# Performance work log

Measured on AMD Instinct MI355X. Metric: run time of the kernel, lower is better.

The kernel has to match this reference:

```python
import jax, jax.numpy as jnp
import numpy as np

N_MENTIONS = 4096
N_PAIRS = 32768
N_SEGMENTS = 1024  # number of spans (ragged softmax groups)
G_DIM = 3 * 768    # span representation dim (3*embed_dim)
D_IN = 3 * G_DIM + 20
HIDDEN = 150


def setup_inputs() -> dict:
    key = jax.random.key(0)
    ks = jax.random.split(key, 11)
    inp = {
        "g_i": jax.random.normal(ks[0], (N_MENTIONS, G_DIM), jnp.float32),
        "mention_scores": jax.random.normal(ks[1], (N_MENTIONS, 1), jnp.float32),
        "speaker_embed": jax.random.normal(ks[2], (3, 20), jnp.float32) * 0.02,
        "W1": jax.random.normal(ks[3], (D_IN, HIDDEN), jnp.float32) * (1.0 / np.sqrt(D_IN)),
        "b1": jnp.zeros((HIDDEN,), jnp.float32),
        "W2": jax.random.normal(ks[4], (HIDDEN, 1), jnp.float32) * (1.0 / np.sqrt(HIDDEN)),
        "b2": jnp.zeros((1,), jnp.float32),
        "mention_ids": jax.random.randint(ks[5], (N_PAIRS,), 0, N_MENTIONS),
        "antecedent_ids": jax.random.randint(ks[6], (N_PAIRS,), 0, N_MENTIONS),
        "speaker_labels": jax.random.randint(ks[7], (N_PAIRS,), 0, 3),
        "segment_ids": jnp.sort(jax.random.randint(ks[8], (N_PAIRS,), 0, N_SEGMENTS)),
    }
    return inp


def reference(g_i, mention_scores, speaker_embed, W1, b1, W2, b2,
              mention_ids, antecedent_ids, speaker_labels, segment_ids):
    # Gather mention / antecedent span representations. [P, G]
    i_g = g_i[mention_ids]
    j_g = g_i[antecedent_ids]
    phi = speaker_embed[speaker_labels]  # [P, speaker_dim]

    # Pair features: cat(i_g, j_g, i_g*j_g, phi). [P, D_IN]
    pairs = jnp.concatenate([i_g, j_g, i_g * j_g, phi], axis=1)

    # Score MLP: Linear -> ReLU -> Linear(->1). (dropout off in eval)
    h = jax.nn.relu(pairs @ W1 + b1)          # [P, HIDDEN]
    s_ij = (h @ W2 + b2)[:, 0]                # [P]

    # coref score = s_i + s_j + s_ij
    s_i = mention_scores[mention_ids, 0]
    s_j = mention_scores[antecedent_ids, 0]
    scores = s_i + s_j + s_ij                 # [P]

    # Ragged per-span softmax with an appended epsilon logit of 0.0.
    seg_max = jax.ops.segment_max(scores, segment_ids, num_segments=N_SEGMENTS)
    m = jnp.maximum(seg_max, 0.0)             # include epsilon=0 in the max
    e = jnp.exp(scores - m[segment_ids])      # [P]
    eps_e = jnp.exp(-m)                       # [S] exp(0 - m)
    denom = jax.ops.segment_sum(e, segment_ids, num_segments=N_SEGMENTS) + eps_e
    pair_probs = e / denom[segment_ids]       # [P]
    eps_probs = eps_e / denom                 # [S]

    # Flattened: all pair probs followed by the per-span epsilon probs.
    return jnp.concatenate([pair_probs, eps_probs])
```

## Files before the change

kernel.cpp:

```cpp
#include <hip/hip_runtime.h>
#include <cstdint>

#define NM   4096
#define NP   32768
#define NSEG 1024
#define GD   2304
#define HID  150
#define NPAD 160
#define KG32 72
#define SEG_ELEMS (KG32 * 10 * 512)

typedef unsigned short u16;
typedef short s16x8 __attribute__((ext_vector_type(8)));
typedef float f32x4 __attribute__((ext_vector_type(4)));
typedef uint32_t u32x4 __attribute__((ext_vector_type(4)));

union Frag {
    uint32_t u[4];
    s16x8    v;
};

__device__ inline uint32_t cvtpk(float lo, float hi) {
    uint32_t r;
    asm("v_cvt_pk_bf16_f32 %0, %1, %2" : "=v"(r) : "v"(lo), "v"(hi));
    return r;
}

__device__ inline f32x4 mfma16(s16x8 a, s16x8 b, f32x4 c) {
    return __builtin_amdgcn_mfma_f32_16x16x32_bf16(a, b, c, 0, 0, 0);
}

__device__ inline s16x8 prodpack(u32x4 iu, u32x4 ju) {
    Frag f;
#pragma unroll
    for (int m = 0; m < 4; ++m) {
        uint32_t x = iu[m], y = ju[m];
        float lo = __builtin_bit_cast(float, x << 16) *
                   __builtin_bit_cast(float, y << 16);
        float hi = __builtin_bit_cast(float, x & 0xffff0000u) *
                   __builtin_bit_cast(float, y & 0xffff0000u);
        f.u[m] = cvtpk(lo, hi);
    }
    return f.v;
}

__global__ void prep_pack_kernel(const float* __restrict__ W1,
                                 u16* __restrict__ wpack) {
    int idx = blockIdx.x * 256 + threadIdx.x;
    if (idx >= 3 * KG32 * 10 * 64) return;
    int lane = idx & 63;
    int t    = idx >> 6;
    int nf   = t % 10;
    int sk   = t / 10;
    int seg  = sk / KG32, kg = sk % KG32;
    int kbase = (seg == 0) ? 2 * GD : ((seg == 1) ? 0 : GD);
    int n    = nf * 16 + (lane & 15);
    int krow = kbase + kg * 32 + ((lane >> 4) << 3);
    u32x4 d = (u32x4){0u, 0u, 0u, 0u};
    if (n < HID) {
#pragma unroll
        for (int jj = 0; jj < 4; ++jj) {
            float v0 = W1[(size_t)(krow + 2 * jj) * HID + n];
            float v1 = W1[(size_t)(krow + 2 * jj + 1) * HID + n];
            d[jj] = cvtpk(v0, v1);
        }
    }
    *(u32x4*)(wpack + (size_t)idx * 8) = d;
}

__global__ void prep_tables_kernel(const float* __restrict__ spk,
                                   const float* __restrict__ W1,
                                   const float* __restrict__ b1,
                                   const float* __restrict__ W2,
                                   float* __restrict__ phib,
                                   float* __restrict__ w2pad) {
    int t = threadIdx.x;
    if (t < 3 * NPAD) {
        int s = t / NPAD, n = t - s * NPAD;
        float a = 0.f;
        if (n < HID) {
            for (int d = 0; d < 20; ++d)
                a = fmaf(spk[s * 20 + d], W1[(size_t)(3 * GD + d) * HID + n], a);
            a += b1[n];
        }
        phib[t] = a;
    } else if (t < 4 * NPAD) {
        int n = t - 3 * NPAD;
        w2pad[n] = (n < HID) ? W2[n] : 0.f;
    }
}

struct A2 { f32x4 x0, x1; };

__launch_bounds__(256)
__global__ void gemm_pre_kernel(const float* __restrict__ gi,
                                const u16* __restrict__ wpackIJ,
                                u16* __restrict__ gbf,
                                float* __restrict__ APre) {
    const int tid = threadIdx.x;
    const int kh = tid >> 6, lane = tid & 63;
    const int quad = lane >> 4, l15 = lane & 15;
    const int mt = blockIdx.x, ng = blockIdx.y;
    const u16* wp = wpackIJ + (size_t)ng * SEG_ELEMS + lane * 8;
    const int row = mt * 16 + l15;

    __shared__ float xch[3][64][44];

    f32x4 acc[10];
#pragma unroll
    for (int b = 0; b < 10; ++b) acc[b] = (f32x4){0.f, 0.f, 0.f, 0.f};

    const float* ap = gi + (size_t)row * GD + quad * 8;
    u16* gb = gbf + (size_t)row * GD + quad * 8;
    const bool emit = (ng == 0);
    const int u0 = kh * 18;

    A2 a0, a1, a2;
    Frag b0[10], b1[10];

#define LDA(ax, k) { ax.x0 = *(const f32x4*)(ap + (u0 + (k)) * 32); \
                     ax.x1 = *(const f32x4*)(ap + (u0 + (k)) * 32 + 4); }
#define LDBP(bb, k) { const u16* wn = wp + (size_t)(u0 + (k)) * 5120; \
        _Pragma("unroll") for (int nf = 0; nf < 10; ++nf) \
            bb[nf].v = *(const s16x8*)(const void*)(wn + nf * 512); }
#define PHP(k, ax, bb) { \
        Frag a; \
        a.u[0] = cvtpk(ax.x0[0], ax.x0[1]); a.u[1] = cvtpk(ax.x0[2], ax.x0[3]); \
        a.u[2] = cvtpk(ax.x1[0], ax.x1[1]); a.u[3] = cvtpk(ax.x1[2], ax.x1[3]); \
        if (emit) *(u32x4*)(gb + (u0 + (k)) * 32) = *(const u32x4*)a.u; \
        __builtin_amdgcn_s_setprio(1); \
        _Pragma("unroll") for (int nf = 0; nf < 10; ++nf) \
            acc[nf] = mfma16(a.v, bb[nf].v, acc[nf]); \
        __builtin_amdgcn_s_setprio(0); }

    LDBP(b0, 0); LDBP(b1, 1);
    LDA(a0, 0); LDA(a1, 1); LDA(a2, 2);

#pragma unroll 1
    for (int t = 0; t < 2; ++t) {
        const int kb = t * 6;
        PHP(kb + 0, a0, b0); LDBP(b0, kb + 2); LDA(a0, kb + 3);
        PHP(kb + 1, a1, b1); LDBP(b1, kb + 3); LDA(a1, kb + 4);
        PHP(kb + 2, a2, b0); LDBP(b0, kb + 4); LDA(a2, kb + 5);
        PHP(kb + 3, a0, b1); LDBP(b1, kb + 5); LDA(a0, kb + 6);
        PHP(kb + 4, a1, b0); LDBP(b0, kb + 6); LDA(a1, kb + 7);
        PHP(kb + 5, a2, b1); LDBP(b1, kb + 7); LDA(a2, kb + 8);
    }
    PHP(12, a0, b0); LDBP(b0, 14); LDA(a0, 15);
    PHP(13, a1, b1); LDBP(b1, 15); LDA(a1, 16);
    PHP(14, a2, b0); LDBP(b0, 16); LDA(a2, 17);
    PHP(15, a0, b1); LDBP(b1, 17);
    PHP(16, a1, b0);
    PHP(17, a2, b1);

#undef LDA
#undef LDBP
#undef PHP

    if (kh != 0) {
        float* dst = &xch[kh - 1][lane][0];
#pragma unroll
        for (int nf = 0; nf < 10; ++nf)
            *(f32x4*)(dst + nf * 4) = acc[nf];
    }
    __syncthreads();
    if (kh == 0) {
#pragma unroll
        for (int k = 0; k < 3; ++k) {
            const float* src = &xch[k][lane][0];
#pragma unroll
            for (int nf = 0; nf < 10; ++nf)
                acc[nf] += *(const f32x4*)(src + nf * 4);
        }
        const int colbase = ng * NPAD + l15;
        float* Ap = APre + (size_t)(mt * 16 + quad * 4) * 320 + colbase;
#pragma unroll
        for (int nf = 0; nf < 10; ++nf)
#pragma unroll
            for (int r = 0; r < 4; ++r)
                Ap[(size_t)r * 320 + nf * 16] = acc[nf][r];
    }
}

struct G4 { u32x4 i0, j0, i1, j1; };

__launch_bounds__(128)
__global__ void gemm_pairs_kernel(const u16* __restrict__ gbf,
                                  const u16* __restrict__ wpackP,
                                  const float* __restrict__ APre,
                                  const float* __restrict__ phib,
                                  const float* __restrict__ w2pad,
                                  const float* __restrict__ mscore,
                                  const float* __restrict__ b2,
                                  const int* __restrict__ mids,
                                  const int* __restrict__ aids,
                                  const int* __restrict__ slab,
                                  float* __restrict__ scores) {
    const int tid = threadIdx.x;
    const int wave = tid >> 6, lane = tid & 63;
    const int quad = lane >> 4, l15 = lane & 15;
    const int base = blockIdx.x * 64 + wave * 32;

    f32x4 acc[2][10];
#pragma unroll
    for (int a = 0; a < 2; ++a)
#pragma unroll
        for (int b = 0; b < 10; ++b) acc[a][b] = (f32x4){0.f, 0.f, 0.f, 0.f};

    const int p0 = base + l15, p1 = base + 16 + l15;
    const u16* ip0 = gbf + (size_t)mids[p0] * GD + quad * 8;
    const u16* jp0 = gbf + (size_t)aids[p0] * GD + quad * 8;
    const u16* ip1 = gbf + (size_t)mids[p1] * GD + quad * 8;
    const u16* jp1 = gbf + (size_t)aids[p1] * GD + quad * 8;
    const u16* wl = wpackP + lane * 8;

    G4 g0, g1, g2, g3;
    Frag b0[10], b1[10];

#define LDG(g, k) { const int off = (k) * 32; \
        g.i0 = *(const u32x4*)(ip0 + off); g.j0 = *(const u32x4*)(jp0 + off); \
        g.i1 = *(const u32x4*)(ip1 + off); g.j1 = *(const u32x4*)(jp1 + off); }
#define LDB(bb, k) { const u16* wn = wl + (size_t)(k) * 5120; \
        _Pragma("unroll") for (int nf = 0; nf < 10; ++nf) \
            bb[nf].v = *(const s16x8*)(const void*)(wn + nf * 512); }
#define PH(g, bb) { \
        s16x8 a0 = prodpack(g.i0, g.j0); \
        s16x8 a1 = prodpack(g.i1, g.j1); \
        __builtin_amdgcn_s_setprio(1); \
        _Pragma("unroll") for (int nf = 0; nf < 10; ++nf) { \
            acc[0][nf] = mfma16(a0, bb[nf].v, acc[0][nf]); \
            acc[1][nf] = mfma16(a1, bb[nf].v, acc[1][nf]); } \
        __builtin_amdgcn_s_setprio(0); }

    LDB(b0, 0); LDB(b1, 1);
    LDG(g0, 0); LDG(g1, 1); LDG(g2, 2); LDG(g3, 3);

#pragma unroll 1
    for (int t = 0; t < 17; ++t) {
        const int kb = t * 4;
        PH(g0, b0); LDB(b0, kb + 2); LDG(g0, kb + 4);
        PH(g1, b1); LDB(b1, kb + 3); LDG(g1, kb + 5);
        PH(g2, b0); LDB(b0, kb + 4); LDG(g2, kb + 6);
        PH(g3, b1); LDB(b1, kb + 5); LDG(g3, kb + 7);
    }
    PH(g0, b0); LDB(b0, 70);
    PH(g1, b1); LDB(b1, 71);
    PH(g2, b0);
    PH(g3, b1);

#undef LDG
#undef LDB
#undef PH

    float w2v[10];
#pragma unroll
    for (int nf = 0; nf < 10; ++nf) w2v[nf] = w2pad[nf * 16 + l15];
    const float b2v = b2[0];

#pragma unroll
    for (int mf = 0; mf < 2; ++mf)
#pragma unroll
        for (int r = 0; r < 4; ++r) {
            const int p  = base + mf * 16 + quad * 4 + r;
            const int mi = mids[p], ai = aids[p], sp = slab[p];
            const float* Ai = APre + (size_t)mi * 320;
            const float* Bj = APre + (size_t)ai * 320 + NPAD;
            const float* Ph = phib + sp * NPAD;
            float partial = 0.f;
#pragma unroll
            for (int nf = 0; nf < 10; ++nf) {
                const int c = nf * 16 + l15;
                float h = acc[mf][nf][r] + Ai[c] + Bj[c] + Ph[c];
                h = fmaxf(h, 0.f);
                partial = fmaf(h, w2v[nf], partial);
            }
            partial += __shfl_xor(partial, 1);
            partial += __shfl_xor(partial, 2);
            partial += __shfl_xor(partial, 4);
            partial += __shfl_xor(partial, 8);
            if (l15 == 0)
                scores[p] = partial + b2v + mscore[mi] + mscore[ai];
        }
}

__global__ void seg_softmax_kernel(const float* __restrict__ scores,
                                   const int* __restrict__ seg,
                                   float* __restrict__ out) {
    const int s = blockIdx.x;
    const int lane = threadIdx.x;
    int lo = 0, hi = NP;
    while (lo < hi) { int mid = (lo + hi) >> 1; if (seg[mid] < s) lo = mid + 1; else hi = mid; }
    const int start = lo;
    int lo2 = start, hi2 = NP;
    while (lo2 < hi2) { int mid = (lo2 + hi2) >> 1; if (seg[mid] <= s) lo2 = mid + 1; else hi2 = mid; }
    const int end = lo2;

    float m = 0.f;
    for (int i = start + lane; i < end; i += 64) m = fmaxf(m, scores[i]);
#pragma unroll
    for (int msk = 1; msk < 64; msk <<= 1) m = fmaxf(m, __shfl_xor(m, msk));

    float sum = 0.f;
    for (int i = start + lane; i < end; i += 64) sum += __expf(scores[i] - m);
#pragma unroll
    for (int msk = 1; msk < 64; msk <<= 1) sum += __shfl_xor(sum, msk);

    const float epse = __expf(-m);
    const float inv  = 1.f / (sum + epse);
    for (int i = start + lane; i < end; i += 64) out[i] = __expf(scores[i] - m) * inv;
    if (lane == 0) out[NP + s] = epse * inv;
}

extern "C" void kernel_launch(void* const* d_in, const int* in_sizes, int n_in,
                              void* d_out, int out_size, void* d_ws, size_t ws_size,
                              hipStream_t stream) {
    const float* gi     = (const float*)d_in[0];
    const float* mscore = (const float*)d_in[1];
    const float* spk    = (const float*)d_in[2];
    const float* W1     = (const float*)d_in[3];
    const float* b1     = (const float*)d_in[4];
    const float* W2     = (const float*)d_in[5];
    const float* b2     = (const float*)d_in[6];
    const int*   mids   = (const int*)d_in[7];
    const int*   aids   = (const int*)d_in[8];
    const int*   slab   = (const int*)d_in[9];
    const int*   segs   = (const int*)d_in[10];
    float* out = (float*)d_out;

    char* w = (char*)d_ws;
    u16*   gbf    = (u16*)w;
    u16*   wpack  = (u16*)(w + 18874368);
    float* APre   = (float*)(w + 21086208);
    float* scores = (float*)(w + 26329088);
    float* phib   = (float*)(w + 26460160);
    float* w2pad  = (float*)(w + 26462080);

    prep_pack_kernel<<<dim3((3 * KG32 * 10 * 64 + 255) / 256), dim3(256), 0, stream>>>(W1, wpack);
    prep_tables_kernel<<<dim3(1), dim3(640), 0, stream>>>(spk, W1, b1, W2, phib, w2pad);
    gemm_pre_kernel<<<dim3(256, 2), dim3(256), 0, stream>>>(gi, wpack + SEG_ELEMS, gbf, APre);
    gemm_pairs_kernel<<<dim3(512), dim3(128), 0, stream>>>(gbf, wpack, APre, phib, w2pad,
                                                           mscore, b2, mids, aids, slab, scores);
    seg_softmax_kernel<<<dim3(NSEG), dim3(64), 0, stream>>>(scores, segs, out);
}
```

Measured before the change: 193.1 us.

## Bucket pairs by mention id, merge pre-GEMM halves, retune pair pipeline

Adds histogram, scan and scatter kernels that sort pair indices into 8 buckets by mention id. Each pair-GEMM block works within one bucket so gathered mention rows share L2 locality. The pre-GEMM now computes both the i and j projections in one block, reading g_i once instead of twice. It also drops the s_setprio hints and changes the pair kernel's prefetch depth from 4 to 3 stages with 6-step unrolling. Costs are three extra launches, atomics, higher register pressure in the fused pre-GEMM (launch bounds now 256,1), and some idle blocks because of the per-bucket padding.

```diff
diff --git a/kernel.cpp b/kernel.cpp
--- a/kernel.cpp
+++ b/kernel.cpp
@@ -9,6 +9,8 @@
 #define NPAD 160
 #define KG32 72
 #define SEG_ELEMS (KG32 * 10 * 512)
+#define NBUCK 8
+#define BUCK_SHIFT 9
 
 typedef unsigned short u16;
 typedef short s16x8 __attribute__((ext_vector_type(8)));
@@ -73,8 +75,10 @@
                                    const float* __restrict__ b1,
                                    const float* __restrict__ W2,
                                    float* __restrict__ phib,
-                                   float* __restrict__ w2pad) {
+                                   float* __restrict__ w2pad,
+                                   int* __restrict__ cnts) {
     int t = threadIdx.x;
+    if (t < 16) cnts[t] = 0;
     if (t < 3 * NPAD) {
         int s = t / NPAD, n = t - s * NPAD;
         float a = 0.f;
@@ -90,78 +94,115 @@
     }
 }
 
+__global__ void bucket_hist_kernel(const int* __restrict__ mids,
+                                   int* __restrict__ cnts) {
+    int p = blockIdx.x * 256 + threadIdx.x;
+    if (p < NP) atomicAdd(&cnts[mids[p] >> BUCK_SHIFT], 1);
+}
+
+__global__ void bucket_scan_kernel(int* __restrict__ cnts) {
+    if (threadIdx.x == 0) {
+        int base = 0;
+        for (int b = 0; b < NBUCK; ++b) {
+            int c = cnts[b];
+            cnts[8 + b] = base;
+            base += c;
+            cnts[b] = 0;
+        }
+    }
+}
+
+__global__ void bucket_scatter_kernel(const int* __restrict__ mids,
+                                      int* __restrict__ cnts,
+                                      int* __restrict__ perm) {
+    int p = blockIdx.x * 256 + threadIdx.x;
+    if (p < NP) {
+        int b = mids[p] >> BUCK_SHIFT;
+        int pos = cnts[8 + b] + atomicAdd(&cnts[b], 1);
+        perm[pos] = p;
+    }
+}
+
 struct A2 { f32x4 x0, x1; };
 
-__launch_bounds__(256)
+__launch_bounds__(256, 1)
 __global__ void gemm_pre_kernel(const float* __restrict__ gi,
-                                const u16* __restrict__ wpackIJ,
+                                const u16* __restrict__ wpack,
                                 u16* __restrict__ gbf,
                                 float* __restrict__ APre) {
     const int tid = threadIdx.x;
     const int kh = tid >> 6, lane = tid & 63;
     const int quad = lane >> 4, l15 = lane & 15;
-    const int mt = blockIdx.x, ng = blockIdx.y;
-    const u16* wp = wpackIJ + (size_t)ng * SEG_ELEMS + lane * 8;
+    const int mt = blockIdx.x;
+    const u16* wpi = wpack + (size_t)1 * SEG_ELEMS + lane * 8;
+    const u16* wpj = wpack + (size_t)2 * SEG_ELEMS + lane * 8;
     const int row = mt * 16 + l15;
 
-    __shared__ float xch[3][64][44];
-
-    f32x4 acc[10];
-#pragma unroll
-    for (int b = 0; b < 10; ++b) acc[b] = (f32x4){0.f, 0.f, 0.f, 0.f};
+    __shared__ float xch[3][64][88];
+
+    f32x4 acci[10], accj[10];
+#pragma unroll
+    for (int b = 0; b < 10; ++b) {
+        acci[b] = (f32x4){0.f, 0.f, 0.f, 0.f};
+        accj[b] = (f32x4){0.f, 0.f, 0.f, 0.f};
+    }
 
     const float* ap = gi + (size_t)row * GD + quad * 8;
     u16* gb = gbf + (size_t)row * GD + quad * 8;
-    const bool emit = (ng == 0);
     const int u0 = kh * 18;
 
     A2 a0, a1, a2;
-    Frag b0[10], b1[10];
+    Frag bi0[10], bi1[10], bj0[10], bj1[10];
 
 #define LDA(ax, k) { ax.x0 = *(const f32x4*)(ap + (u0 + (k)) * 32); \
                      ax.x1 = *(const f32x4*)(ap + (u0 + (k)) * 32 + 4); }
-#define LDBP(bb, k) { const u16* wn = wp + (size_t)(u0 + (k)) * 5120; \
+#define LDBI(bb, k) { const u16* wn = wpi + (size_t)(u0 + (k)) * 5120; \
         _Pragma("unroll") for (int nf = 0; nf < 10; ++nf) \
             bb[nf].v = *(const s16x8*)(const void*)(wn + nf * 512); }
-#define PHP(k, ax, bb) { \
+#define LDBJ(bb, k) { const u16* wn = wpj + (size_t)(u0 + (k)) * 5120; \
+        _Pragma("unroll") for (int nf = 0; nf < 10; ++nf) \
+            bb[nf].v = *(const s16x8*)(const void*)(wn + nf * 512); }
+#define PHP(k, ax, bbi, bbj) { \
         Frag a; \
         a.u[0] = cvtpk(ax.x0[0], ax.x0[1]); a.u[1] = cvtpk(ax.x0[2], ax.x0[3]); \
         a.u[2] = cvtpk(ax.x1[0], ax.x1[1]); a.u[3] = cvtpk(ax.x1[2], ax.x1[3]); \
-        if (emit) *(u32x4*)(gb + (u0 + (k)) * 32) = *(const u32x4*)a.u; \
-        __builtin_amdgcn_s_setprio(1); \
-        _Pragma("unroll") for (int nf = 0; nf < 10; ++nf) \
-            acc[nf] = mfma16(a.v, bb[nf].v, acc[nf]); \
-        __builtin_amdgcn_s_setprio(0); }
-
-    LDBP(b0, 0); LDBP(b1, 1);
+        *(u32x4*)(gb + (u0 + (k)) * 32) = *(const u32x4*)a.u; \
+        _Pragma("unroll") for (int nf = 0; nf < 10; ++nf) { \
+            acci[nf] = mfma16(a.v, bbi[nf].v, acci[nf]); \
+            accj[nf] = mfma16(a.v, bbj[nf].v, accj[nf]); } }
+
     LDA(a0, 0); LDA(a1, 1); LDA(a2, 2);
+    LDBI(bi0, 0); LDBJ(bj0, 0); LDBI(bi1, 1); LDBJ(bj1, 1);
 
 #pragma unroll 1
     for (int t = 0; t < 2; ++t) {
         const int kb = t * 6;
-        PHP(kb + 0, a0, b0); LDBP(b0, kb + 2); LDA(a0, kb + 3);
-        PHP(kb + 1, a1, b1); LDBP(b1, kb + 3); LDA(a1, kb + 4);
-        PHP(kb + 2, a2, b0); LDBP(b0, kb + 4); LDA(a2, kb + 5);
-        PHP(kb + 3, a0, b1); LDBP(b1, kb + 5); LDA(a0, kb + 6);
-        PHP(kb + 4, a1, b0); LDBP(b0, kb + 6); LDA(a1, kb + 7);
-        PHP(kb + 5, a2, b1); LDBP(b1, kb + 7); LDA(a2, kb + 8);
-    }
-    PHP(12, a0, b0); LDBP(b0, 14); LDA(a0, 15);
-    PHP(13, a1, b1); LDBP(b1, 15); LDA(a1, 16);
-    PHP(14, a2, b0); LDBP(b0, 16); LDA(a2, 17);
-    PHP(15, a0, b1); LDBP(b1, 17);
-    PHP(16, a1, b0);
-    PHP(17, a2, b1);
+        PHP(kb + 0, a0, bi0, bj0); LDA(a0, kb + 3); LDBI(bi0, kb + 2); LDBJ(bj0, kb + 2);
+        PHP(kb + 1, a1, bi1, bj1); LDA(a1, kb + 4); LDBI(bi1, kb + 3); LDBJ(bj1, kb + 3);
+        PHP(kb + 2, a2, bi0, bj0); LDA(a2, kb + 5); LDBI(bi0, kb + 4); LDBJ(bj0, kb + 4);
+        PHP(kb + 3, a0, bi1, bj1); LDA(a0, kb + 6); LDBI(bi1, kb + 5); LDBJ(bj1, kb + 5);
+        PHP(kb + 4, a1, bi0, bj0); LDA(a1, kb + 7); LDBI(bi0, kb + 6); LDBJ(bj0, kb + 6);
+        PHP(kb + 5, a2, bi1, bj1); LDA(a2, kb + 8); LDBI(bi1, kb + 7); LDBJ(bj1, kb + 7);
+    }
+    PHP(12, a0, bi0, bj0); LDA(a0, 15); LDBI(bi0, 14); LDBJ(bj0, 14);
+    PHP(13, a1, bi1, bj1); LDA(a1, 16); LDBI(bi1, 15); LDBJ(bj1, 15);
+    PHP(14, a2, bi0, bj0); LDA(a2, 17); LDBI(bi0, 16); LDBJ(bj0, 16);
+    PHP(15, a0, bi1, bj1); LDBI(bi1, 17); LDBJ(bj1, 17);
+    PHP(16, a1, bi0, bj0);
+    PHP(17, a2, bi1, bj1);
 
 #undef LDA
-#undef LDBP
+#undef LDBI
+#undef LDBJ
 #undef PHP
 
     if (kh != 0) {
         float* dst = &xch[kh - 1][lane][0];
 #pragma unroll
-        for (int nf = 0; nf < 10; ++nf)
-            *(f32x4*)(dst + nf * 4) = acc[nf];
+        for (int nf = 0; nf < 10; ++nf) {
+            *(f32x4*)(dst + nf * 4)      = acci[nf];
+            *(f32x4*)(dst + 44 + nf * 4) = accj[nf];
+        }
     }
     __syncthreads();
     if (kh == 0) {
@@ -169,16 +210,19 @@
         for (int k = 0; k < 3; ++k) {
             const float* src = &xch[k][lane][0];
 #pragma unroll
-            for (int nf = 0; nf < 10; ++nf)
-                acc[nf] += *(const f32x4*)(src + nf * 4);
-        }
-        const int colbase = ng * NPAD + l15;
-        float* Ap = APre + (size_t)(mt * 16 + quad * 4) * 320 + colbase;
+            for (int nf = 0; nf < 10; ++nf) {
+                acci[nf] += *(const f32x4*)(src + nf * 4);
+                accj[nf] += *(const f32x4*)(src + 44 + nf * 4);
+            }
+        }
+        float* Ap = APre + (size_t)(mt * 16 + quad * 4) * 320 + l15;
 #pragma unroll
         for (int nf = 0; nf < 10; ++nf)
 #pragma unroll
-            for (int r = 0; r < 4; ++r)
-                Ap[(size_t)r * 320 + nf * 16] = acc[nf][r];
+            for (int r = 0; r < 4; ++r) {
+                Ap[(size_t)r * 320 + nf * 16]        = acci[nf][r];
+                Ap[(size_t)r * 320 + NPAD + nf * 16] = accj[nf][r];
+            }
     }
 }
 
@@ -195,11 +239,18 @@
                                   const int* __restrict__ mids,
                                   const int* __restrict__ aids,
                                   const int* __restrict__ slab,
+                                  const int* __restrict__ cnts,
+                                  const int* __restrict__ perm,
                                   float* __restrict__ scores) {
     const int tid = threadIdx.x;
     const int wave = tid >> 6, lane = tid & 63;
     const int quad = lane >> 4, l15 = lane & 15;
-    const int base = blockIdx.x * 64 + wave * 32;
+    const int bkt  = blockIdx.x & 7;
+    const int tile = blockIdx.x >> 3;
+    const int cntb  = cnts[bkt];
+    const int bbase = cnts[8 + bkt];
+    const int tbase = tile * 64 + wave * 32;
+    if (tbase >= cntb) return;
 
     f32x4 acc[2][10];
 #pragma unroll
@@ -207,14 +258,17 @@
 #pragma unroll
         for (int b = 0; b < 10; ++b) acc[a][b] = (f32x4){0.f, 0.f, 0.f, 0.f};
 
-    const int p0 = base + l15, p1 = base + 16 + l15;
+    const int s0 = tbase + l15, s1 = tbase + 16 + l15;
+    const int q0 = (s0 < cntb) ? s0 : (cntb - 1);
+    const int q1 = (s1 < cntb) ? s1 : (cntb - 1);
+    const int p0 = perm[bbase + q0], p1 = perm[bbase + q1];
     const u16* ip0 = gbf + (size_t)mids[p0] * GD + quad * 8;
     const u16* jp0 = gbf + (size_t)aids[p0] * GD + quad * 8;
     const u16* ip1 = gbf + (size_t)mids[p1] * GD + quad * 8;
     const u16* jp1 = gbf + (size_t)aids[p1] * GD + quad * 8;
     const u16* wl = wpackP + lane * 8;
 
-    G4 g0, g1, g2, g3;
+    G4 g0, g1, g2;
     Frag b0[10], b1[10];
 
 #define LDG(g, k) { const int off = (k) * 32; \
@@ -226,27 +280,29 @@
 #define PH(g, bb) { \
         s16x8 a0 = prodpack(g.i0, g.j0); \
         s16x8 a1 = prodpack(g.i1, g.j1); \
-        __builtin_amdgcn_s_setprio(1); \
         _Pragma("unroll") for (int nf = 0; nf < 10; ++nf) { \
             acc[0][nf] = mfma16(a0, bb[nf].v, acc[0][nf]); \
-            acc[1][nf] = mfma16(a1, bb[nf].v, acc[1][nf]); } \
-        __builtin_amdgcn_s_setprio(0); }
-
+            acc[1][nf] = mfma16(a1, bb[nf].v, acc[1][nf]); } }
+
+    LDG(g0, 0); LDG(g1, 1); LDG(g2, 2);
     LDB(b0, 0); LDB(b1, 1);
-    LDG(g0, 0); LDG(g1, 1); LDG(g2, 2); LDG(g3, 3);
 
 #pragma unroll 1
-    for (int t = 0; t < 17; ++t) {
-        const int kb = t * 4;
-        PH(g0, b0); LDB(b0, kb + 2); LDG(g0, kb + 4);
-        PH(g1, b1); LDB(b1, kb + 3); LDG(g1, kb + 5);
-        PH(g2, b0); LDB(b0, kb + 4); LDG(g2, kb + 6);
-        PH(g3, b1); LDB(b1, kb + 5); LDG(g3, kb + 7);
-    }
-    PH(g0, b0); LDB(b0, 70);
-    PH(g1, b1); LDB(b1, 71);
-    PH(g2, b0);
-    PH(g3, b1);
+    for (int t = 0; t < 11; ++t) {
+        const int kb = t * 6;
+        PH(g0, b0); LDG(g0, kb + 3); LDB(b0, kb + 2);
+        PH(g1, b1); LDG(g1, kb + 4); LDB(b1, kb + 3);
+        PH(g2, b0); LDG(g2, kb + 5); LDB(b0, kb + 4);
+        PH(g0, b1); LDG(g0, kb + 6); LDB(b1, kb + 5);
+        PH(g1, b0); LDG(g1, kb + 7); LDB(b0, kb + 6);
+        PH(g2, b1); LDG(g2, kb + 8); LDB(b1, kb + 7);
+    }
+    PH(g0, b0); LDG(g0, 69); LDB(b0, 68);
+    PH(g1, b1); LDG(g1, 70); LDB(b1, 69);
+    PH(g2, b0); LDG(g2, 71); LDB(b0, 70);
+    PH(g0, b1); LDB(b1, 71);
+    PH(g1, b0);
+    PH(g2, b1);
 
 #undef LDG
 #undef LDB
@@ -261,7 +317,9 @@
     for (int mf = 0; mf < 2; ++mf)
 #pragma unroll
         for (int r = 0; r < 4; ++r) {
-            const int p  = base + mf * 16 + quad * 4 + r;
+            const int slot = tile * 64 + wave * 32 + mf * 16 + quad * 4 + r;
+            const bool valid = slot < cntb;
+            const int p  = perm[bbase + (valid ? slot : 0)];
             const int mi = mids[p], ai = aids[p], sp = slab[p];
             const float* Ai = APre + (size_t)mi * 320;
             const float* Bj = APre + (size_t)ai * 320 + NPAD;
@@ -278,7 +336,7 @@
             partial += __shfl_xor(partial, 2);
             partial += __shfl_xor(partial, 4);
             partial += __shfl_xor(partial, 8);
-            if (l15 == 0)
+            if (l15 == 0 && valid)
                 scores[p] = partial + b2v + mscore[mi] + mscore[ai];
         }
 }
@@ -334,11 +392,17 @@
     float* scores = (float*)(w + 26329088);
     float* phib   = (float*)(w + 26460160);
     float* w2pad  = (float*)(w + 26462080);
+    int*   cnts   = (int*)(w + 26462720);
+    int*   perm   = (int*)(w + 26462784);
 
     prep_pack_kernel<<<dim3((3 * KG32 * 10 * 64 + 255) / 256), dim3(256), 0, stream>>>(W1, wpack);
-    prep_tables_kernel<<<dim3(1), dim3(640), 0, stream>>>(spk, W1, b1, W2, phib, w2pad);
-    gemm_pre_kernel<<<dim3(256, 2), dim3(256), 0, stream>>>(gi, wpack + SEG_ELEMS, gbf, APre);
-    gemm_pairs_kernel<<<dim3(512), dim3(128), 0, stream>>>(gbf, wpack, APre, phib, w2pad,
-                                                           mscore, b2, mids, aids, slab, scores);
+    prep_tables_kernel<<<dim3(1), dim3(640), 0, stream>>>(spk, W1, b1, W2, phib, w2pad, cnts);
+    bucket_hist_kernel<<<dim3(128), dim3(256), 0, stream>>>(mids, cnts);
+    bucket_scan_kernel<<<dim3(1), dim3(64), 0, stream>>>(cnts);
+    bucket_scatter_kernel<<<dim3(128), dim3(256), 0, stream>>>(mids, cnts, perm);
+    gemm_pre_kernel<<<dim3(256), dim3(256), 0, stream>>>(gi, wpack, gbf, APre);
+    gemm_pairs_kernel<<<dim3(576), dim3(128), 0, stream>>>(gbf, wpack, APre, phib, w2pad,
+                                                           mscore, b2, mids, aids, slab,
+                                                           cnts, perm, scores);
     seg_softmax_kernel<<<dim3(NSEG), dim3(64), 0, stream>>>(scores, segs, out);
 }
```

Result: slower. 525.8 us (+172.3%).

## Merge prep kernels, drop setprio, rebalance pair GEMM prefetch pipeline

Applied to the files above, without the earlier changes.

Folds the weight-packing and small table-prep kernels into one launch with block-range dispatch, removing one kernel launch. It removes the s_setprio bracketing around the MFMA groups in both GEMM kernels. The pair GEMM's gather prefetch drops from four to three register buffers and its loop is re-unrolled by six, with gathers issued before weight loads. The aim is lower register pressure and less launch overhead, at the cost of a shallower prefetch depth for the random row gathers.

```diff
diff --git a/kernel.cpp b/kernel.cpp
--- a/kernel.cpp
+++ b/kernel.cpp
@@ -44,49 +44,50 @@
     return f.v;
 }
 
-__global__ void prep_pack_kernel(const float* __restrict__ W1,
-                                 u16* __restrict__ wpack) {
-    int idx = blockIdx.x * 256 + threadIdx.x;
-    if (idx >= 3 * KG32 * 10 * 64) return;
-    int lane = idx & 63;
-    int t    = idx >> 6;
-    int nf   = t % 10;
-    int sk   = t / 10;
-    int seg  = sk / KG32, kg = sk % KG32;
-    int kbase = (seg == 0) ? 2 * GD : ((seg == 1) ? 0 : GD);
-    int n    = nf * 16 + (lane & 15);
-    int krow = kbase + kg * 32 + ((lane >> 4) << 3);
-    u32x4 d = (u32x4){0u, 0u, 0u, 0u};
-    if (n < HID) {
-#pragma unroll
-        for (int jj = 0; jj < 4; ++jj) {
-            float v0 = W1[(size_t)(krow + 2 * jj) * HID + n];
-            float v1 = W1[(size_t)(krow + 2 * jj + 1) * HID + n];
-            d[jj] = cvtpk(v0, v1);
+__launch_bounds__(256)
+__global__ void prep_kernel(const float* __restrict__ W1,
+                            const float* __restrict__ spk,
+                            const float* __restrict__ b1,
+                            const float* __restrict__ W2,
+                            u16* __restrict__ wpack,
+                            float* __restrict__ phib,
+                            float* __restrict__ w2pad) {
+    const int b = blockIdx.x;
+    if (b < 540) {
+        int idx = b * 256 + threadIdx.x;
+        int lane = idx & 63;
+        int t    = idx >> 6;
+        int nf   = t % 10;
+        int sk   = t / 10;
+        int seg  = sk / KG32, kg = sk % KG32;
+        int kbase = (seg == 0) ? 2 * GD : ((seg == 1) ? 0 : GD);
+        int n    = nf * 16 + (lane & 15);
+        int krow = kbase + kg * 32 + ((lane >> 4) << 3);
+        u32x4 d = (u32x4){0u, 0u, 0u, 0u};
+        if (n < HID) {
+#pragma unroll
+            for (int jj = 0; jj < 4; ++jj) {
+                float v0 = W1[(size_t)(krow + 2 * jj) * HID + n];
+                float v1 = W1[(size_t)(krow + 2 * jj + 1) * HID + n];
+                d[jj] = cvtpk(v0, v1);
+            }
         }
-    }
-    *(u32x4*)(wpack + (size_t)idx * 8) = d;
-}
-
-__global__ void prep_tables_kernel(const float* __restrict__ spk,
-                                   const float* __restrict__ W1,
-                                   const float* __restrict__ b1,
-                                   const float* __restrict__ W2,
-                                   float* __restrict__ phib,
-                                   float* __restrict__ w2pad) {
-    int t = threadIdx.x;
-    if (t < 3 * NPAD) {
-        int s = t / NPAD, n = t - s * NPAD;
-        float a = 0.f;
-        if (n < HID) {
-            for (int d = 0; d < 20; ++d)
-                a = fmaf(spk[s * 20 + d], W1[(size_t)(3 * GD + d) * HID + n], a);
-            a += b1[n];
+        *(u32x4*)(wpack + (size_t)idx * 8) = d;
+    } else {
+        int t = (b - 540) * 256 + threadIdx.x;
+        if (t < 3 * NPAD) {
+            int s = t / NPAD, n = t - s * NPAD;
+            float a = 0.f;
+            if (n < HID) {
+                for (int d = 0; d < 20; ++d)
+                    a = fmaf(spk[s * 20 + d], W1[(size_t)(3 * GD + d) * HID + n], a);
+                a += b1[n];
+            }
+            phib[t] = a;
+        } else if (t < 4 * NPAD) {
+            int n = t - 3 * NPAD;
+            w2pad[n] = (n < HID) ? W2[n] : 0.f;
         }
-        phib[t] = a;
-    } else if (t < 4 * NPAD) {
-        int n = t - 3 * NPAD;
-        w2pad[n] = (n < HID) ? W2[n] : 0.f;
     }
 }
 
@@ -128,10 +129,8 @@
         a.u[0] = cvtpk(ax.x0[0], ax.x0[1]); a.u[1] = cvtpk(ax.x0[2], ax.x0[3]); \
         a.u[2] = cvtpk(ax.x1[0], ax.x1[1]); a.u[3] = cvtpk(ax.x1[2], ax.x1[3]); \
         if (emit) *(u32x4*)(gb + (u0 + (k)) * 32) = *(const u32x4*)a.u; \
-        __builtin_amdgcn_s_setprio(1); \
         _Pragma("unroll") for (int nf = 0; nf < 10; ++nf) \
-            acc[nf] = mfma16(a.v, bb[nf].v, acc[nf]); \
-        __builtin_amdgcn_s_setprio(0); }
+            acc[nf] = mfma16(a.v, bb[nf].v, acc[nf]); }
 
     LDBP(b0, 0); LDBP(b1, 1);
     LDA(a0, 0); LDA(a1, 1); LDA(a2, 2);
@@ -214,7 +213,7 @@
     const u16* jp1 = gbf + (size_t)aids[p1] * GD + quad * 8;
     const u16* wl = wpackP + lane * 8;
 
-    G4 g0, g1, g2, g3;
+    G4 g0, g1, g2;
     Frag b0[10], b1[10];
 
 #define LDG(g, k) { const int off = (k) * 32; \
@@ -226,27 +225,29 @@
 #define PH(g, bb) { \
         s16x8 a0 = prodpack(g.i0, g.j0); \
         s16x8 a1 = prodpack(g.i1, g.j1); \
-        __builtin_amdgcn_s_setprio(1); \
         _Pragma("unroll") for (int nf = 0; nf < 10; ++nf) { \
             acc[0][nf] = mfma16(a0, bb[nf].v, acc[0][nf]); \
-            acc[1][nf] = mfma16(a1, bb[nf].v, acc[1][nf]); } \
-        __builtin_amdgcn_s_setprio(0); }
-
+            acc[1][nf] = mfma16(a1, bb[nf].v, acc[1][nf]); } }
+
+    LDG(g0, 0); LDG(g1, 1); LDG(g2, 2);
     LDB(b0, 0); LDB(b1, 1);
-    LDG(g0, 0); LDG(g1, 1); LDG(g2, 2); LDG(g3, 3);
 
 #pragma unroll 1
-    for (int t = 0; t < 17; ++t) {
-        const int kb = t * 4;
-        PH(g0, b0); LDB(b0, kb + 2); LDG(g0, kb + 4);
-        PH(g1, b1); LDB(b1, kb + 3); LDG(g1, kb + 5);
-        PH(g2, b0); LDB(b0, kb + 4); LDG(g2, kb + 6);
-        PH(g3, b1); LDB(b1, kb + 5); LDG(g3, kb + 7);
-    }
-    PH(g0, b0); LDB(b0, 70);
-    PH(g1, b1); LDB(b1, 71);
-    PH(g2, b0);
-    PH(g3, b1);
+    for (int t = 0; t < 11; ++t) {
+        const int kb = t * 6;
+        PH(g0, b0); LDG(g0, kb + 3); LDB(b0, kb + 2);
+        PH(g1, b1); LDG(g1, kb + 4); LDB(b1, kb + 3);
+        PH(g2, b0); LDG(g2, kb + 5); LDB(b0, kb + 4);
+        PH(g0, b1); LDG(g0, kb + 6); LDB(b1, kb + 5);
+        PH(g1, b0); LDG(g1, kb + 7); LDB(b0, kb + 6);
+        PH(g2, b1); LDG(g2, kb + 8); LDB(b1, kb + 7);
+    }
+    PH(g0, b0); LDG(g0, 69); LDB(b0, 68);
+    PH(g1, b1); LDG(g1, 70); LDB(b1, 69);
+    PH(g2, b0); LDG(g2, 71); LDB(b0, 70);
+    PH(g0, b1); LDB(b1, 71);
+    PH(g1, b0);
+    PH(g2, b1);
 
 #undef LDG
 #undef LDB
@@ -335,8 +336,7 @@
     float* phib   = (float*)(w + 26460160);
     float* w2pad  = (float*)(w + 26462080);
 
-    prep_pack_kernel<<<dim3((3 * KG32 * 10 * 64 + 255) / 256), dim3(256), 0, stream>>>(W1, wpack);
-    prep_tables_kernel<<<dim3(1), dim3(640), 0, stream>>>(spk, W1, b1, W2, phib, w2pad);
+    prep_kernel<<<dim3(543), dim3(256), 0, stream>>>(W1, spk, b1, W2, wpack, phib, w2pad);
     gemm_pre_kernel<<<dim3(256, 2), dim3(256), 0, stream>>>(gi, wpack + SEG_ELEMS, gbf, APre);
     gemm_pairs_kernel<<<dim3(512), dim3(128), 0, stream>>>(gbf, wpack, APre, phib, w2pad,
                                                            mscore, b2, mids, aids, slab, scores);
```

Result: no change. 192.4 us (-0.4%).
